# Optimization experiments

Measured on AMD Instinct MI355X. Metric: run time of the kernel, lower is better.

Reference implementation:

```python
import jax, jax.numpy as jnp
import numpy as np

B, N, K, D, H, FF, L, NH = 8, 50, 20, 3, 128, 2048, 3, 8
S = N * K
HD = H // NH


def setup_inputs() -> dict:
    key = jax.random.key(0)
    ks = jax.random.split(key, 16)
    visited = jax.random.uniform(ks[0], (B, S)) < 0.05
    # the single most-recent action per batch row (status flips 0 -> 1)
    action_idx = jax.random.randint(ks[1], (B,), 0, S)
    visited = visited.at[jnp.arange(B), action_idx].set(True)
    feats = jax.random.normal(ks[2], (B, S, D - 1)) * visited[:, :, None]
    state = jnp.concatenate([feats, visited[:, :, None].astype(jnp.float32)], axis=-1)
    prev_state = state.at[jnp.arange(B), action_idx, :].set(0.0)

    def w(k, shape, s=0.02):
        return jax.random.normal(k, shape, dtype=jnp.float32) * s

    return dict(
        prev_state=prev_state, state=state,
        W_pre=w(ks[3], (D, H)), b_pre=jnp.zeros(H),
        Wq=w(ks[4], (L, H, H)), bq=jnp.zeros((L, H)),
        Wk=w(ks[5], (L, H, H)), bk=jnp.zeros((L, H)),
        Wv=w(ks[6], (L, H, H)), bv=jnp.zeros((L, H)),
        Wo=w(ks[7], (L, H, H)), bo=jnp.zeros((L, H)),
        ln1_g=jnp.ones((L, H)), ln1_b=jnp.zeros((L, H)),
        Wff1=w(ks[8], (L, H, FF)), bff1=jnp.zeros((L, FF)),
        Wff2=w(ks[9], (L, FF, H)), bff2=jnp.zeros((L, H)),
        ln2_g=jnp.ones((L, H)), ln2_b=jnp.zeros((L, H)),
        W_comb=w(ks[10], (2 * H, H)), b_comb=jnp.zeros(H),
        W_dec=w(ks[11], (H, H)), b_dec=jnp.zeros(H),
        W_lin=w(ks[12], (S, S)), b_lin=jnp.zeros(S),
    )


def _layer_norm(x, g, b, eps=1e-5):
    m = jnp.mean(x, -1, keepdims=True)
    v = jnp.mean(jnp.square(x - m), -1, keepdims=True)
    return (x - m) * jax.lax.rsqrt(v + eps) * g + b


def _update_mask(state):
    # vectorized equivalent of the original Python-loop scatter mask
    status = state[:, :, -1] != 0                      # visited [B, S], S = K*N channel-major
    mask = status
    vis_kn = status.reshape(B, K, N)
    user_any = vis_kn.any(axis=1)                      # [B, N]: user visited on any channel
    mask = mask | jnp.broadcast_to(user_any[:, None, :], (B, K, N)).reshape(B, S)
    assigned = state.reshape(B, K, N, D).sum(-1) != 0  # [B, K, N]
    full = assigned.sum(-1) >= 2                       # [B, K]: channel already has 2 users
    mask = mask | jnp.broadcast_to(full[:, :, None], (B, K, N)).reshape(B, S)
    return mask


def reference(prev_state, state, W_pre, b_pre, Wq, bq, Wk, bk, Wv, bv, Wo, bo,
              ln1_g, ln1_b, Wff1, bff1, Wff2, bff2, ln2_g, ln2_b,
              W_comb, b_comb, W_dec, b_dec, W_lin, b_lin):
    mask = _update_mask(state)
    # exactly one status change per batch row (sequential RL step)
    diff = prev_state[:, :, -1] != state[:, :, -1]
    act_idx = jnp.argmax(diff, axis=1)                 # [B]

    x = state @ W_pre + b_pre                          # [B, S, H]
    scale = np.float32(1.0 / np.sqrt(HD))
    for i in range(L):  # 3 post-LN transformer encoder layers
        q = (x @ Wq[i] + bq[i]).reshape(B, S, NH, HD)
        k = (x @ Wk[i] + bk[i]).reshape(B, S, NH, HD)
        v = (x @ Wv[i] + bv[i]).reshape(B, S, NH, HD)
        att = jax.nn.softmax(jnp.einsum('bqhd,bkhd->bhqk', q, k) * scale, axis=-1)
        o = jnp.einsum('bhqk,bkhd->bqhd', att, v).reshape(B, S, H) @ Wo[i] + bo[i]
        x = _layer_norm(x + o, ln1_g[i], ln1_b[i])
        ff = jax.nn.relu(x @ Wff1[i] + bff1[i]) @ Wff2[i] + bff2[i]
        x = _layer_norm(x + ff, ln2_g[i], ln2_b[i])

    last = x[jnp.arange(B), act_idx]                   # [B, H]
    combined = jnp.concatenate([x.mean(axis=1), last], axis=-1)  # [B, 2H]
    g = combined @ W_comb + b_comb                     # [B, H]
    dec = x @ W_dec + b_dec                            # [B, S, H]
    scores = jnp.einsum('bsh,bh->bs', dec, g)          # [B, S]
    masked = scores @ W_lin + b_lin                    # Q-Learning head
    return jnp.where(mask, -jnp.inf, masked)
```

## Files before the change

### kernel.cpp

```cpp
#include <hip/hip_runtime.h>
#include <math.h>

#define Bb 8
#define Ss 1000
#define Kk 20
#define Nn 50
#define Dd 3
#define Hh 128
#define FFf 2048
#define Ll 3
#define NHh 8
#define HDd 16
#define ROWS (Bb*Ss)

#define SENTINEL -3.0e38f

typedef unsigned short ush;
typedef short short8 __attribute__((ext_vector_type(8)));
typedef float f32x4 __attribute__((ext_vector_type(4)));

__device__ __forceinline__ ush f2b(float f) {
  unsigned x = __float_as_uint(f);
  return (ush)((x + 0x7fff + ((x >> 16) & 1)) >> 16);
}

__global__ __launch_bounds__(256) void mask_kernel(const float* __restrict__ state,
                                                   const float* __restrict__ prev_state,
                                                   int* __restrict__ mask, int* __restrict__ act_idx) {
  int b = blockIdx.x, tid = threadIdx.x;
  __shared__ unsigned char status[Ss], assigned[Ss], uany[Nn], fullk[Kk];
  __shared__ int act;
  if (tid == 0) act = 1 << 30;
  __syncthreads();
  for (int s = tid; s < Ss; s += 256) {
    const float* st = state + ((size_t)b * Ss + s) * Dd;
    float f2 = st[2];
    status[s] = (f2 != 0.f);
    assigned[s] = ((st[0] + st[1] + f2) != 0.f);
    float p2 = prev_state[((size_t)b * Ss + s) * Dd + 2];
    if (p2 != f2) atomicMin(&act, s);
  }
  __syncthreads();
  if (tid < Nn) {
    unsigned char a = 0;
    for (int k = 0; k < Kk; ++k) a |= status[k * Nn + tid];
    uany[tid] = a;
  } else if (tid >= 64 && tid < 64 + Kk) {
    int k = tid - 64, cnt = 0;
    for (int n = 0; n < Nn; ++n) cnt += assigned[k * Nn + n];
    fullk[k] = (cnt >= 2);
  }
  __syncthreads();
  for (int s = tid; s < Ss; s += 256)
    mask[b * Ss + s] = (int)(status[s] | uany[s % Nn] | fullk[s / Nn]);
  if (tid == 0) act_idx[b] = (act >= Ss) ? 0 : act;
}

__global__ __launch_bounds__(256) void pre_kernel(const float* __restrict__ state,
                                                  const float* __restrict__ W_pre,
                                                  const float* __restrict__ b_pre,
                                                  float* __restrict__ x, ush* __restrict__ xbf) {
  int idx = blockIdx.x * 256 + threadIdx.x;
  if (idx >= ROWS * Hh) return;
  int row = idx >> 7, n = idx & 127;
  const float* st = state + (size_t)row * Dd;
  float v = b_pre[n] + st[0] * W_pre[n] + st[1] * W_pre[Hh + n] + st[2] * W_pre[2 * Hh + n];
  x[idx] = v;
  xbf[idx] = f2b(v);
}

#define S1 (384*128)
#define S2 (128*128)
#define S3 (2048*128)
#define S4 (128*2048)
#define SPL (S1+S2+S3+S4)
__global__ __launch_bounds__(256) void wprep_kernel(const float* __restrict__ Wq, const float* __restrict__ Wk,
                                                    const float* __restrict__ Wv, const float* __restrict__ Wo,
                                                    const float* __restrict__ Wff1, const float* __restrict__ Wff2,
                                                    const float* __restrict__ bq, const float* __restrict__ bk,
                                                    const float* __restrict__ bv, const float* __restrict__ W_dec,
                                                    ush* __restrict__ wqkvT, ush* __restrict__ woT,
                                                    ush* __restrict__ wff1T, ush* __restrict__ wff2T,
                                                    float* __restrict__ bqkv, float* __restrict__ wdecT) {
  int idx = blockIdx.x * 256 + threadIdx.x;
  if (idx < Ll * SPL) {
    int l = idx / SPL, r = idx % SPL;
    if (r < S1) {
      int k = r / 384, n = r % 384;
      float v = (n < 128) ? Wq[((size_t)l * Hh + k) * Hh + n]
              : (n < 256) ? Wk[((size_t)l * Hh + k) * Hh + (n - 128)]
                          : Wv[((size_t)l * Hh + k) * Hh + (n - 256)];
      wqkvT[((size_t)l * 384 + n) * 128 + k] = f2b(v);
    } else if (r < S1 + S2) {
      int rr = r - S1; int k = rr >> 7, n = rr & 127;
      woT[((size_t)l * 128 + n) * 128 + k] = f2b(Wo[((size_t)l * Hh + k) * Hh + n]);
    } else if (r < S1 + S2 + S3) {
      int rr = r - S1 - S2; int k = rr >> 11, n = rr & 2047;
      wff1T[((size_t)l * 2048 + n) * 128 + k] = f2b(Wff1[((size_t)l * Hh + k) * FFf + n]);
    } else {
      int rr = r - S1 - S2 - S3; int k = rr >> 7, n = rr & 127;
      wff2T[((size_t)l * 128 + n) * 2048 + k] = f2b(Wff2[((size_t)l * FFf + k) * Hh + n]);
    }
  }
  if (idx < Ll * 384) {
    int l = idx / 384, c = idx % 384;
    bqkv[idx] = (c < 128) ? bq[l * Hh + c] : (c < 256 ? bk[l * Hh + c - 128] : bv[l * Hh + c - 256]);
  }
  if (idx < Hh * Hh) {
    int k = idx >> 7, n = idx & 127;
    wdecT[(size_t)n * Hh + k] = W_dec[idx];
  }
}

#define LDP 40
template <int RELU, int QKVV>
__global__ __launch_bounds__(256) void gemm_mfma(const ush* __restrict__ A, const ush* __restrict__ Wt,
                                                 const float* __restrict__ bias, ush* __restrict__ out,
                                                 int N, int K, ush* __restrict__ vTout) {
  __shared__ ush As[2][64 * LDP];
  __shared__ ush Bs[2][64 * LDP];
  int tid = threadIdx.x;
  int lane = tid & 63, wid = tid >> 6;
  int wr = wid >> 1, wc = wid & 1;
  int m0 = blockIdx.y * 64, n0 = blockIdx.x * 64;
  int lrow = tid >> 2, lk = (tid & 3) << 3;
  int quad = lane >> 4, l16 = lane & 15, kb = quad << 3;

  const ush* Ap = A + (size_t)(m0 + lrow) * K + lk;
  const ush* Bp = Wt + (size_t)(n0 + lrow) * K + lk;

  f32x4 acc[2][2];
#pragma unroll
  for (int i = 0; i < 2; ++i)
#pragma unroll
    for (int j = 0; j < 2; ++j) acc[i][j] = (f32x4){0.f, 0.f, 0.f, 0.f};

  short8 pa = *(const short8*)Ap;
  short8 pb = *(const short8*)Bp;
  *(short8*)&As[0][lrow * LDP + lk] = pa;
  *(short8*)&Bs[0][lrow * LDP + lk] = pb;
  __syncthreads();

  int NT = K >> 5;
  for (int it = 0; it < NT; ++it) {
    int cur = it & 1;
    bool have = (it + 1 < NT);
    if (have) {
      pa = *(const short8*)(Ap + (it + 1) * 32);
      pb = *(const short8*)(Bp + (it + 1) * 32);
    }
    short8 a0 = *(short8*)&As[cur][(wr * 32 + l16) * LDP + kb];
    short8 a1 = *(short8*)&As[cur][(wr * 32 + 16 + l16) * LDP + kb];
    short8 b0 = *(short8*)&Bs[cur][(wc * 32 + l16) * LDP + kb];
    short8 b1 = *(short8*)&Bs[cur][(wc * 32 + 16 + l16) * LDP + kb];
    acc[0][0] = __builtin_amdgcn_mfma_f32_16x16x32_bf16(a0, b0, acc[0][0], 0, 0, 0);
    acc[0][1] = __builtin_amdgcn_mfma_f32_16x16x32_bf16(a0, b1, acc[0][1], 0, 0, 0);
    acc[1][0] = __builtin_amdgcn_mfma_f32_16x16x32_bf16(a1, b0, acc[1][0], 0, 0, 0);
    acc[1][1] = __builtin_amdgcn_mfma_f32_16x16x32_bf16(a1, b1, acc[1][1], 0, 0, 0);
    if (have) {
      *(short8*)&As[cur ^ 1][lrow * LDP + lk] = pa;
      *(short8*)&Bs[cur ^ 1][lrow * LDP + lk] = pb;
    }
    __syncthreads();
  }

#pragma unroll
  for (int i = 0; i < 2; ++i)
#pragma unroll
    for (int j = 0; j < 2; ++j) {
      int col = n0 + wc * 32 + j * 16 + l16;
      int rbase = m0 + wr * 32 + i * 16 + quad * 4;
      float bval = bias[col];
#pragma unroll
      for (int v = 0; v < 4; ++v) {
        float o = acc[i][j][v] + bval;
        if (RELU) o = fmaxf(o, 0.f);
        if (QKVV && col >= 256) {
          int row = rbase + v;
          int bb2 = row / 1000, qq = row - bb2 * 1000;
          vTout[((size_t)(bb2 * 128 + (col - 256))) * 1024 + qq] = f2b(o);
        } else {
          out[(size_t)(rbase + v) * N + col] = f2b(o);
        }
      }
    }
}

#define F2P 72
template <int KK>
__global__ __launch_bounds__(256) void gemm_ln_kernel(const ush* __restrict__ A,
                                                      const ush* __restrict__ Wt,
                                                      const float* __restrict__ bias,
                                                      const float* __restrict__ ln_g, const float* __restrict__ ln_b,
                                                      float* __restrict__ x, ush* __restrict__ xbf) {
  __shared__ ush As[2][32 * F2P];
  __shared__ ush Bs[2][128 * F2P];
  __shared__ float red1[2][2][16], red2[2][2][16];
  __shared__ float pbias[128], pg[128], pb[128];

  int tid = threadIdx.x, lane = tid & 63, w = tid >> 6;
  int wr = w & 1, wc = w >> 1;
  int l16 = lane & 15, quad = lane >> 4, kb = quad * 8;
  int m0 = blockIdx.x * 32;
  if (tid < 128) { pbias[tid] = bias[tid]; pg[tid] = ln_g[tid]; pb[tid] = ln_b[tid]; }

  f32x4 acc[4];
#pragma unroll
  for (int j = 0; j < 4; ++j) acc[j] = (f32x4){0.f, 0.f, 0.f, 0.f};

  int arow = tid >> 3, alk = (tid & 7) << 3;
  const ush* Ap = A + (size_t)(m0 + arow) * KK + alk;
  const ush* Bp = Wt + (size_t)arow * KK + alk;

  short8 pa = *(const short8*)Ap;
  short8 pbr[4];
#pragma unroll
  for (int rep = 0; rep < 4; ++rep)
    pbr[rep] = *(const short8*)(Bp + (size_t)rep * 32 * KK);
  *(short8*)&As[0][arow * F2P + alk] = pa;
#pragma unroll
  for (int rep = 0; rep < 4; ++rep)
    *(short8*)&Bs[0][(rep * 32 + arow) * F2P + alk] = pbr[rep];
  __syncthreads();

  const int NT = KK / 64;
  for (int it = 0; it < NT; ++it) {
    int cur = it & 1;
    bool have = (it + 1 < NT);
    if (have) {
      pa = *(const short8*)(Ap + (it + 1) * 64);
#pragma unroll
      for (int rep = 0; rep < 4; ++rep)
        pbr[rep] = *(const short8*)(Bp + (size_t)rep * 32 * KK + (it + 1) * 64);
    }
#pragma unroll
    for (int kk = 0; kk < 2; ++kk) {
      short8 a = *(short8*)&As[cur][(wr * 16 + l16) * F2P + kk * 32 + kb];
#pragma unroll
      for (int j = 0; j < 4; ++j) {
        short8 b = *(short8*)&Bs[cur][(wc * 64 + j * 16 + l16) * F2P + kk * 32 + kb];
        acc[j] = __builtin_amdgcn_mfma_f32_16x16x32_bf16(a, b, acc[j], 0, 0, 0);
      }
    }
    if (have) {
      *(short8*)&As[cur ^ 1][arow * F2P + alk] = pa;
#pragma unroll
      for (int rep = 0; rep < 4; ++rep)
        *(short8*)&Bs[cur ^ 1][(rep * 32 + arow) * F2P + alk] = pbr[rep];
    }
    __syncthreads();
  }

  float v[4][4], s1[4] = {0.f, 0.f, 0.f, 0.f}, s2[4] = {0.f, 0.f, 0.f, 0.f};
#pragma unroll
  for (int j = 0; j < 4; ++j) {
    int col = wc * 64 + j * 16 + l16;
#pragma unroll
    for (int r = 0; r < 4; ++r) {
      int row = m0 + wr * 16 + quad * 4 + r;
      float vv = acc[j][r] + pbias[col] + x[(size_t)row * Hh + col];
      v[j][r] = vv; s1[r] += vv; s2[r] += vv * vv;
    }
  }
#pragma unroll
  for (int m = 1; m <= 8; m <<= 1) {
#pragma unroll
    for (int r = 0; r < 4; ++r) { s1[r] += __shfl_xor(s1[r], m); s2[r] += __shfl_xor(s2[r], m); }
  }
  if (l16 == 0) {
#pragma unroll
    for (int r = 0; r < 4; ++r) {
      red1[wr][wc][quad * 4 + r] = s1[r];
      red2[wr][wc][quad * 4 + r] = s2[r];
    }
  }
  __syncthreads();
#pragma unroll
  for (int r = 0; r < 4; ++r) {
    int qr = quad * 4 + r;
    float t1 = red1[wr][0][qr] + red1[wr][1][qr];
    float t2 = red2[wr][0][qr] + red2[wr][1][qr];
    float mean = t1 * (1.f / 128.f);
    float var = t2 * (1.f / 128.f) - mean * mean;
    float rstd = rsqrtf(var + 1e-5f);
    int row = m0 + wr * 16 + quad * 4 + r;
#pragma unroll
    for (int j = 0; j < 4; ++j) {
      int col = wc * 64 + j * 16 + l16;
      float o = (v[j][r] - mean) * rstd * pg[col] + pb[col];
      size_t gi = (size_t)row * Hh + col;
      x[gi] = o; xbf[gi] = f2b(o);
    }
  }
}

__global__ __launch_bounds__(256) void attn_mfma(const ush* __restrict__ qkv,
                                                 const ush* __restrict__ vT,
                                                 ush* __restrict__ attn_o) {
  int blk = blockIdx.x;
  int local = blk >> 3;
  int bh = ((blk & 7) << 3) | (local >> 4);
  int qt = local & 15;
  int b = bh >> 3, h = bh & 7;
  int qbase = qt * 64;
  int tid = threadIdx.x, lane = tid & 63, w = tid >> 6;
  int l16 = lane & 15, quad = lane >> 4, kb = quad * 8;

  __shared__ ush Ks[2][64][40];
  __shared__ ush Vs[2][16][72];
  __shared__ ush Pb[4][16][72];

  if (tid < 128) {
    int row = tid >> 1, g = tid & 1;
    *(short8*)&Ks[0][row][16 + g * 8] = (short8){0, 0, 0, 0, 0, 0, 0, 0};
    *(short8*)&Ks[1][row][16 + g * 8] = (short8){0, 0, 0, 0, 0, 0, 0, 0};
  }

  int qrow = qbase + w * 16 + l16; if (qrow >= Ss) qrow = Ss - 1;
  short8 aq = *(const short8*)(qkv + (size_t)(b * Ss + qrow) * 384 + h * HDd + kb);

  int srow = tid >> 1, sg = tid & 1;
  int sd = (tid - 128) >> 3, skg = (tid - 128) & 7;
  const ush* kbase = qkv + (size_t)b * Ss * 384 + 128 + h * HDd;
  const ush* vbase = vT + (size_t)(b * 128 + h * 16) * 1024;

  if (tid < 128) {
    short8 s8 = (short8){0, 0, 0, 0, 0, 0, 0, 0};
    if (srow < Ss) s8 = *(const short8*)(kbase + (size_t)srow * 384 + sg * 8);
    *(short8*)&Ks[0][srow][sg * 8] = s8;
  } else {
    *(short8*)&Vs[0][sd][skg * 8] = *(const short8*)(vbase + (size_t)sd * 1024 + skg * 8);
  }
  __syncthreads();

  const short one_b = (short)0x3F80;
  const short8 ones = (short8){one_b, one_b, one_b, one_b, one_b, one_b, one_b, one_b};
  f32x4 acc_pv = (f32x4){0.f, 0.f, 0.f, 0.f};
  f32x4 acc_l = (f32x4){0.f, 0.f, 0.f, 0.f};
  const f32x4 zero4 = (f32x4){0.f, 0.f, 0.f, 0.f};

  for (int it = 0; it < 16; ++it) {
    int k0 = it * 64;
    int cur = it & 1, nxt = cur ^ 1;
    bool have = (it + 1 < 16);

    short8 gk, gv;
    if (have) {
      if (tid < 128) {
        gk = (short8){0, 0, 0, 0, 0, 0, 0, 0};
        int key = k0 + 64 + srow;
        if (key < Ss) gk = *(const short8*)(kbase + (size_t)key * 384 + sg * 8);
      } else {
        gv = *(const short8*)(vbase + (size_t)sd * 1024 + k0 + 64 + skg * 8);
      }
    }

    bool tail = (k0 + 64 > Ss);
#pragma unroll
    for (int kn = 0; kn < 4; ++kn) {
      short8 ak = *(short8*)&Ks[cur][kn * 16 + l16][kb];
      f32x4 s = __builtin_amdgcn_mfma_f32_16x16x32_bf16(ak, aq, zero4, 0, 0, 0);
      float p0 = __expf(s[0] * 0.25f);
      float p1 = __expf(s[1] * 0.25f);
      float p2 = __expf(s[2] * 0.25f);
      float p3 = __expf(s[3] * 0.25f);
      if (tail) {
        int keyb = k0 + kn * 16 + quad * 4;
        if (keyb + 0 >= Ss) p0 = 0.f;
        if (keyb + 1 >= Ss) p1 = 0.f;
        if (keyb + 2 >= Ss) p2 = 0.f;
        if (keyb + 3 >= Ss) p3 = 0.f;
      }
      unsigned lo, hi;
      asm("v_cvt_pk_bf16_f32 %0, %1, %2" : "=v"(lo) : "v"(p0), "v"(p1));
      asm("v_cvt_pk_bf16_f32 %0, %1, %2" : "=v"(hi) : "v"(p2), "v"(p3));
      *(uint2*)&Pb[w][l16][kn * 16 + quad * 4] = make_uint2(lo, hi);
    }

    short8 pa0 = *(short8*)&Pb[w][l16][kb];
    short8 pa1 = *(short8*)&Pb[w][l16][32 + kb];
    short8 vb0 = *(short8*)&Vs[cur][l16][kb];
    short8 vb1 = *(short8*)&Vs[cur][l16][32 + kb];
    acc_pv = __builtin_amdgcn_mfma_f32_16x16x32_bf16(pa0, vb0, acc_pv, 0, 0, 0);
    acc_pv = __builtin_amdgcn_mfma_f32_16x16x32_bf16(pa1, vb1, acc_pv, 0, 0, 0);
    acc_l = __builtin_amdgcn_mfma_f32_16x16x32_bf16(pa0, ones, acc_l, 0, 0, 0);
    acc_l = __builtin_amdgcn_mfma_f32_16x16x32_bf16(pa1, ones, acc_l, 0, 0, 0);

    if (have) {
      if (tid < 128) *(short8*)&Ks[nxt][srow][sg * 8] = gk;
      else *(short8*)&Vs[nxt][sd][skg * 8] = gv;
    }
    __syncthreads();
  }

#pragma unroll
  for (int r = 0; r < 4; ++r) {
    int q = qbase + w * 16 + quad * 4 + r;
    if (q < Ss)
      attn_o[((size_t)(b * Ss + q)) * Hh + h * HDd + l16] = f2b(acc_pv[r] / acc_l[r]);
  }
}

__global__ __launch_bounds__(128) void mean_part_kernel(const float* __restrict__ x,
                                                        float* __restrict__ mpart) {
  int c = blockIdx.x, b = blockIdx.y, n = threadIdx.x;
  const float* xb = x + ((size_t)b * Ss + c * 125) * Hh + n;
  float s = 0.f;
#pragma unroll 5
  for (int i = 0; i < 125; ++i) s += xb[(size_t)i * Hh];
  mpart[(c * Bb + b) * Hh + n] = s;
}

__global__ __launch_bounds__(128) void ghc_kernel(const float* __restrict__ x, const float* __restrict__ mpart,
                                                  const int* __restrict__ act_idx,
                                                  const float* __restrict__ W_comb, const float* __restrict__ b_comb,
                                                  const float* __restrict__ wdecT, const float* __restrict__ b_dec,
                                                  float* __restrict__ h, float* __restrict__ cb) {
  int b = blockIdx.x, n = threadIdx.x;
  __shared__ float cs[2 * Hh], gs[Hh], red[2];
  float mean = 0.f;
#pragma unroll
  for (int c = 0; c < 8; ++c) mean += mpart[(c * Bb + b) * Hh + n];
  cs[n] = mean * (1.f / Ss);
  cs[Hh + n] = x[((size_t)b * Ss + act_idx[b]) * Hh + n];
  __syncthreads();
  float acc = b_comb[n];
  for (int j = 0; j < 2 * Hh; ++j) acc += cs[j] * W_comb[(size_t)j * Hh + n];
  gs[n] = acc;
  __syncthreads();
  float hv = 0.f;
  for (int c = 0; c < Hh; ++c) hv += wdecT[(size_t)c * Hh + n] * gs[c];
  h[b * Hh + n] = hv;
  float t = b_dec[n] * gs[n];
  for (int off = 32; off; off >>= 1) t += __shfl_down(t, off);
  if ((n & 63) == 0) red[n >> 6] = t;
  __syncthreads();
  if (n == 0) cb[b] = red[0] + red[1];
}

__global__ __launch_bounds__(256) void scores_kernel(const float* __restrict__ x, const float* __restrict__ h,
                                                     const float* __restrict__ cb, float* __restrict__ scores) {
  int wid = threadIdx.x >> 6, lane = threadIdx.x & 63;
  int row = blockIdx.x * 4 + wid;
  if (row >= ROWS) return;
  int b = row / Ss;
  const float* xr = x + (size_t)row * Hh;
  const float* hb = h + b * Hh;
  float s = xr[lane] * hb[lane] + xr[lane + 64] * hb[lane + 64];
  for (int off = 32; off; off >>= 1) s += __shfl_down(s, off);
  if (lane == 0) scores[row] = s + cb[b];
}

__global__ __launch_bounds__(256) void final_part(const float* __restrict__ scores,
                                                  const float* __restrict__ W_lin,
                                                  float* __restrict__ fpart) {
  int spc = blockIdx.x, kc = blockIdx.y;
  int tid = threadIdx.x;
  __shared__ float ss[8][125];
  for (int i = tid; i < 8 * 125; i += 256) {
    int bb = i / 125, s = i - bb * 125;
    ss[bb][s] = scores[bb * Ss + kc * 125 + s];
  }
  __syncthreads();
  if (tid < 250) {
    int sp = spc * 250 + tid;
    float acc[8];
#pragma unroll
    for (int bb = 0; bb < 8; ++bb) acc[bb] = 0.f;
    const float* wl = &W_lin[(size_t)(kc * 125) * Ss + sp];
#pragma unroll 5
    for (int s = 0; s < 125; ++s) {
      float wv = wl[(size_t)s * Ss];
#pragma unroll
      for (int bb = 0; bb < 8; ++bb) acc[bb] = fmaf(ss[bb][s], wv, acc[bb]);
    }
#pragma unroll
    for (int bb = 0; bb < 8; ++bb)
      fpart[((size_t)kc * Bb + bb) * Ss + sp] = acc[bb];
  }
}

__global__ __launch_bounds__(256) void final_combine(const float* __restrict__ fpart,
                                                     const float* __restrict__ b_lin,
                                                     const int* __restrict__ mask,
                                                     float* __restrict__ out) {
  int b = blockIdx.y;
  int sp = blockIdx.x * 256 + threadIdx.x;
  if (sp >= Ss) return;
  float acc = b_lin[sp];
#pragma unroll
  for (int kc = 0; kc < 8; ++kc) acc += fpart[((size_t)kc * Bb + b) * Ss + sp];
  out[b * Ss + sp] = mask[b * Ss + sp] ? SENTINEL : acc;
}

extern "C" void kernel_launch(void* const* d_in, const int* in_sizes, int n_in,
                              void* d_out, int out_size, void* d_ws, size_t ws_size,
                              hipStream_t stream) {
  const float* prev_state = (const float*)d_in[0];
  const float* state = (const float*)d_in[1];
  const float* W_pre = (const float*)d_in[2];
  const float* b_pre = (const float*)d_in[3];
  const float* Wq = (const float*)d_in[4];
  const float* bq = (const float*)d_in[5];
  const float* Wk = (const float*)d_in[6];
  const float* bk = (const float*)d_in[7];
  const float* Wv = (const float*)d_in[8];
  const float* bv = (const float*)d_in[9];
  const float* Wo = (const float*)d_in[10];
  const float* bo = (const float*)d_in[11];
  const float* ln1_g = (const float*)d_in[12];
  const float* ln1_b = (const float*)d_in[13];
  const float* Wff1 = (const float*)d_in[14];
  const float* bff1 = (const float*)d_in[15];
  const float* Wff2 = (const float*)d_in[16];
  const float* bff2 = (const float*)d_in[17];
  const float* ln2_g = (const float*)d_in[18];
  const float* ln2_b = (const float*)d_in[19];
  const float* W_comb = (const float*)d_in[20];
  const float* b_comb = (const float*)d_in[21];
  const float* W_dec = (const float*)d_in[22];
  const float* b_dec = (const float*)d_in[23];
  const float* W_lin = (const float*)d_in[24];
  const float* b_lin = (const float*)d_in[25];

  char* wsp = (char*)d_ws;
  auto alloc = [&](size_t bytes) { char* p = wsp; wsp += (bytes + 255) & ~(size_t)255; return p; };
  int* mask = (int*)alloc(ROWS * 4);
  int* act = (int*)alloc(Bb * 4);
  ush* wqkvT = (ush*)alloc((size_t)Ll * 384 * 128 * 2);
  ush* woT = (ush*)alloc((size_t)Ll * 128 * 128 * 2);
  ush* wff1T = (ush*)alloc((size_t)Ll * 2048 * 128 * 2);
  ush* wff2T = (ush*)alloc((size_t)Ll * 128 * 2048 * 2);
  float* bqkv = (float*)alloc((size_t)Ll * 384 * 4);
  float* wdecT = (float*)alloc((size_t)Hh * Hh * 4);
  float* x = (float*)alloc((size_t)ROWS * Hh * 4);
  ush* xbf = (ush*)alloc((size_t)ROWS * Hh * 2);
  ush* qkv_bf = (ush*)alloc((size_t)ROWS * 384 * 2);
  ush* vT = (ush*)alloc((size_t)Bb * 128 * 1024 * 2);
  ush* attn_ob = (ush*)alloc((size_t)ROWS * Hh * 2);
  float* mpart = (float*)alloc((size_t)8 * Bb * Hh * 4);
  float* hbuf = (float*)alloc((size_t)Bb * Hh * 4);
  float* cb = (float*)alloc((size_t)Bb * 4);
  float* scores = (float*)alloc((size_t)ROWS * 4);
  float* fpart = (float*)alloc((size_t)8 * Bb * Ss * 4);
  ush* ffb = (ush*)alloc((size_t)ROWS * FFf * 2);

  wprep_kernel<<<dim3((Ll * SPL + 255) / 256), 256, 0, stream>>>(Wq, Wk, Wv, Wo, Wff1, Wff2, bq, bk, bv, W_dec,
                                                                 wqkvT, woT, wff1T, wff2T, bqkv, wdecT);
  mask_kernel<<<Bb, 256, 0, stream>>>(state, prev_state, mask, act);
  pre_kernel<<<dim3((ROWS * Hh + 255) / 256), 256, 0, stream>>>(state, W_pre, b_pre, x, xbf);

  for (int l = 0; l < Ll; ++l) {
    gemm_mfma<0, 1><<<dim3(384 / 64, ROWS / 64), 256, 0, stream>>>(
        xbf, wqkvT + (size_t)l * 384 * 128, bqkv + l * 384, qkv_bf, 384, 128, vT);
    attn_mfma<<<dim3(1024), 256, 0, stream>>>(qkv_bf, vT, attn_ob);
    gemm_ln_kernel<128><<<dim3(ROWS / 32), 256, 0, stream>>>(
        attn_ob, woT + (size_t)l * 128 * 128, bo + l * Hh, ln1_g + l * Hh, ln1_b + l * Hh, x, xbf);
    gemm_mfma<1, 0><<<dim3(2048 / 64, ROWS / 64), 256, 0, stream>>>(
        xbf, wff1T + (size_t)l * 2048 * 128, bff1 + l * FFf, ffb, 2048, 128, nullptr);
    gemm_ln_kernel<2048><<<dim3(ROWS / 32), 256, 0, stream>>>(
        ffb, wff2T + (size_t)l * 128 * 2048, bff2 + l * Hh, ln2_g + l * Hh, ln2_b + l * Hh, x, xbf);
  }

  mean_part_kernel<<<dim3(8, Bb), 128, 0, stream>>>(x, mpart);
  ghc_kernel<<<Bb, 128, 0, stream>>>(x, mpart, act, W_comb, b_comb, wdecT, b_dec, hbuf, cb);
  scores_kernel<<<dim3(ROWS / 4), 256, 0, stream>>>(x, hbuf, cb, scores);
  final_part<<<dim3(4, 8), 256, 0, stream>>>(scores, W_lin, fpart);
  final_combine<<<dim3(4, Bb), 256, 0, stream>>>(fpart, b_lin, mask, (float*)d_out);
}
```

Before: 381.2 us.

## Tile weight transposes, vectorize V^T stores, add 16-row out-proj LN kernel, fuse mean

New measurement: 383.5 us. About the same (+0.6%).

```diff
diff --git a/kernel.cpp b/kernel.cpp
--- a/kernel.cpp
+++ b/kernel.cpp
@@ -17,6 +17,7 @@
 
 typedef unsigned short ush;
 typedef short short8 __attribute__((ext_vector_type(8)));
+typedef short short4v __attribute__((ext_vector_type(4)));
 typedef float f32x4 __attribute__((ext_vector_type(4)));
 
 __device__ __forceinline__ ush f2b(float f) {
@@ -59,9 +60,11 @@
 __global__ __launch_bounds__(256) void pre_kernel(const float* __restrict__ state,
                                                   const float* __restrict__ W_pre,
                                                   const float* __restrict__ b_pre,
-                                                  float* __restrict__ x, ush* __restrict__ xbf) {
+                                                  float* __restrict__ x, ush* __restrict__ xbf,
+                                                  float* __restrict__ mpart) {
   int idx = blockIdx.x * 256 + threadIdx.x;
   if (idx >= ROWS * Hh) return;
+  if (idx < Bb * Hh) mpart[idx] = 0.f;
   int row = idx >> 7, n = idx & 127;
   const float* st = state + (size_t)row * Dd;
   float v = b_pre[n] + st[0] * W_pre[n] + st[1] * W_pre[Hh + n] + st[2] * W_pre[2 * Hh + n];
@@ -69,46 +72,67 @@
   xbf[idx] = f2b(v);
 }
 
-#define S1 (384*128)
-#define S2 (128*128)
-#define S3 (2048*128)
-#define S4 (128*2048)
-#define SPL (S1+S2+S3+S4)
-__global__ __launch_bounds__(256) void wprep_kernel(const float* __restrict__ Wq, const float* __restrict__ Wk,
-                                                    const float* __restrict__ Wv, const float* __restrict__ Wo,
-                                                    const float* __restrict__ Wff1, const float* __restrict__ Wff2,
-                                                    const float* __restrict__ bq, const float* __restrict__ bk,
-                                                    const float* __restrict__ bv, const float* __restrict__ W_dec,
-                                                    ush* __restrict__ wqkvT, ush* __restrict__ woT,
-                                                    ush* __restrict__ wff1T, ush* __restrict__ wff2T,
-                                                    float* __restrict__ bqkv, float* __restrict__ wdecT) {
-  int idx = blockIdx.x * 256 + threadIdx.x;
-  if (idx < Ll * SPL) {
-    int l = idx / SPL, r = idx % SPL;
-    if (r < S1) {
-      int k = r / 384, n = r % 384;
-      float v = (n < 128) ? Wq[((size_t)l * Hh + k) * Hh + n]
-              : (n < 256) ? Wk[((size_t)l * Hh + k) * Hh + (n - 128)]
-                          : Wv[((size_t)l * Hh + k) * Hh + (n - 256)];
-      wqkvT[((size_t)l * 384 + n) * 128 + k] = f2b(v);
-    } else if (r < S1 + S2) {
-      int rr = r - S1; int k = rr >> 7, n = rr & 127;
-      woT[((size_t)l * 128 + n) * 128 + k] = f2b(Wo[((size_t)l * Hh + k) * Hh + n]);
-    } else if (r < S1 + S2 + S3) {
-      int rr = r - S1 - S2; int k = rr >> 11, n = rr & 2047;
-      wff1T[((size_t)l * 2048 + n) * 128 + k] = f2b(Wff1[((size_t)l * Hh + k) * FFf + n]);
-    } else {
-      int rr = r - S1 - S2 - S3; int k = rr >> 7, n = rr & 127;
-      wff2T[((size_t)l * 128 + n) * 2048 + k] = f2b(Wff2[((size_t)l * FFf + k) * Hh + n]);
-    }
-  }
-  if (idx < Ll * 384) {
-    int l = idx / 384, c = idx % 384;
-    bqkv[idx] = (c < 128) ? bq[l * Hh + c] : (c < 256 ? bk[l * Hh + c - 128] : bv[l * Hh + c - 256]);
-  }
-  if (idx < Hh * Hh) {
-    int k = idx >> 7, n = idx & 127;
-    wdecT[(size_t)n * Hh + k] = W_dec[idx];
+#define TQKV 144
+#define TWO  48
+#define TFF1 768
+#define TFF2 768
+#define TWD  16
+#define TBIAS 5
+#define TTOT (TQKV+TWO+TFF1+TFF2+TWD+TBIAS)
+__global__ __launch_bounds__(256) void transpose_prep(
+    const float* __restrict__ Wq, const float* __restrict__ Wk, const float* __restrict__ Wv,
+    const float* __restrict__ Wo, const float* __restrict__ Wff1, const float* __restrict__ Wff2,
+    const float* __restrict__ bq, const float* __restrict__ bk, const float* __restrict__ bv,
+    const float* __restrict__ W_dec,
+    ush* __restrict__ wqkvT, ush* __restrict__ woT, ush* __restrict__ wff1T, ush* __restrict__ wff2T,
+    float* __restrict__ bqkv, float* __restrict__ wdecT) {
+  int t = blockIdx.x, tid = threadIdx.x;
+  if (t >= TTOT - TBIAS) {
+    int idx = (t - (TTOT - TBIAS)) * 256 + tid;
+    if (idx < Ll * 384) {
+      int l = idx / 384, c = idx % 384;
+      bqkv[idx] = (c < 128) ? bq[l * Hh + c] : (c < 256 ? bk[l * Hh + c - 128] : bv[l * Hh + c - 256]);
+    }
+    return;
+  }
+  __shared__ float lf[32][33];
+  int tr = tid >> 5, tc = tid & 31;
+  const float* s; ush* d = nullptr; float* df = nullptr;
+  int sp, dp;
+  if (t < TQKV) {
+    int l = t / 48, rem = t % 48, mat = rem / 16, tt = rem % 16;
+    int ti = tt >> 2, tj = tt & 3;
+    const float* m = (mat == 0) ? Wq : (mat == 1) ? Wk : Wv;
+    s = m + (size_t)l * 16384 + (size_t)(ti * 32) * 128 + tj * 32; sp = 128;
+    d = wqkvT + ((size_t)l * 384 + mat * 128 + tj * 32) * 128 + ti * 32; dp = 128;
+  } else if (t < TQKV + TWO) {
+    int r0 = t - TQKV; int l = r0 / 16, tt = r0 % 16, ti = tt >> 2, tj = tt & 3;
+    s = Wo + (size_t)l * 16384 + (size_t)(ti * 32) * 128 + tj * 32; sp = 128;
+    d = woT + ((size_t)l * 128 + tj * 32) * 128 + ti * 32; dp = 128;
+  } else if (t < TQKV + TWO + TFF1) {
+    int r0 = t - TQKV - TWO; int l = r0 / 256, tt = r0 % 256, ti = tt >> 6, tj = tt & 63;
+    s = Wff1 + (size_t)l * 128 * 2048 + (size_t)(ti * 32) * 2048 + tj * 32; sp = 2048;
+    d = wff1T + ((size_t)l * 2048 + tj * 32) * 128 + ti * 32; dp = 128;
+  } else if (t < TQKV + TWO + TFF1 + TFF2) {
+    int r0 = t - TQKV - TWO - TFF1; int l = r0 / 256, tt = r0 % 256, ti = tt >> 2, tj = tt & 3;
+    s = Wff2 + (size_t)l * 2048 * 128 + (size_t)(ti * 32) * 128 + tj * 32; sp = 128;
+    d = wff2T + ((size_t)l * 128 + tj * 32) * 2048 + ti * 32; dp = 2048;
+  } else {
+    int tt = t - TQKV - TWO - TFF1 - TFF2; int ti = tt >> 2, tj = tt & 3;
+    s = W_dec + (size_t)(ti * 32) * 128 + tj * 32; sp = 128;
+    df = wdecT + (size_t)(tj * 32) * 128 + ti * 32; dp = 128;
+  }
+#pragma unroll
+  for (int p = 0; p < 4; ++p) {
+    int r = tr + p * 8;
+    lf[r][tc] = s[(size_t)r * sp + tc];
+  }
+  __syncthreads();
+#pragma unroll
+  for (int p = 0; p < 4; ++p) {
+    int r = tr + p * 8;
+    if (d) d[(size_t)r * dp + tc] = f2b(lf[tc][r]);
+    else   df[(size_t)r * dp + tc] = lf[tc][r];
   }
 }
 
@@ -171,15 +195,17 @@
       int col = n0 + wc * 32 + j * 16 + l16;
       int rbase = m0 + wr * 32 + i * 16 + quad * 4;
       float bval = bias[col];
-#pragma unroll
-      for (int v = 0; v < 4; ++v) {
-        float o = acc[i][j][v] + bval;
-        if (RELU) o = fmaxf(o, 0.f);
-        if (QKVV && col >= 256) {
-          int row = rbase + v;
-          int bb2 = row / 1000, qq = row - bb2 * 1000;
-          vTout[((size_t)(bb2 * 128 + (col - 256))) * 1024 + qq] = f2b(o);
-        } else {
+      if (QKVV && col >= 256) {
+        int bb2 = rbase / 1000, qq = rbase - bb2 * 1000;
+        short4v pk;
+#pragma unroll
+        for (int v = 0; v < 4; ++v) pk[v] = (short)f2b(acc[i][j][v] + bval);
+        *(short4v*)&vTout[((size_t)(bb2 * 128 + (col - 256))) * 1024 + qq] = pk;
+      } else {
+#pragma unroll
+        for (int v = 0; v < 4; ++v) {
+          float o = acc[i][j][v] + bval;
+          if (RELU) o = fmaxf(o, 0.f);
           out[(size_t)(rbase + v) * N + col] = f2b(o);
         }
       }
@@ -187,12 +213,14 @@
 }
 
 #define F2P 72
-template <int KK>
+template <int MEANOUT>
 __global__ __launch_bounds__(256) void gemm_ln_kernel(const ush* __restrict__ A,
                                                       const ush* __restrict__ Wt,
                                                       const float* __restrict__ bias,
                                                       const float* __restrict__ ln_g, const float* __restrict__ ln_b,
-                                                      float* __restrict__ x, ush* __restrict__ xbf) {
+                                                      float* __restrict__ x, ush* __restrict__ xbf,
+                                                      float* __restrict__ mpart) {
+  const int KK = 2048;
   __shared__ ush As[2][32 * F2P];
   __shared__ ush Bs[2][128 * F2P];
   __shared__ float red1[2][2][16], red2[2][2][16];
@@ -275,6 +303,7 @@
     }
   }
   __syncthreads();
+  float osum[4] = {0.f, 0.f, 0.f, 0.f};
 #pragma unroll
   for (int r = 0; r < 4; ++r) {
     int qr = quad * 4 + r;
@@ -287,6 +316,117 @@
 #pragma unroll
     for (int j = 0; j < 4; ++j) {
       int col = wc * 64 + j * 16 + l16;
+      float o = (v[j][r] - mean) * rstd * pg[col] + pb[col];
+      size_t gi = (size_t)row * Hh + col;
+      x[gi] = o; xbf[gi] = f2b(o);
+      if (MEANOUT) osum[j] += o;
+    }
+  }
+  if (MEANOUT) {
+    int gb = (m0 + wr * 16 + quad * 4) / 1000;
+#pragma unroll
+    for (int j = 0; j < 4; ++j)
+      atomicAdd(&mpart[gb * 128 + wc * 64 + j * 16 + l16], osum[j]);
+  }
+}
+
+__global__ __launch_bounds__(256) void gemm_ln16(const ush* __restrict__ A,
+                                                 const ush* __restrict__ Wt,
+                                                 const float* __restrict__ bias,
+                                                 const float* __restrict__ ln_g, const float* __restrict__ ln_b,
+                                                 float* __restrict__ x, ush* __restrict__ xbf) {
+  __shared__ ush As[2][16 * F2P];
+  __shared__ ush Bs[2][128 * F2P];
+  __shared__ float red1[4][16], red2[4][16];
+  __shared__ float pbias[128], pg[128], pb[128];
+
+  int tid = threadIdx.x, lane = tid & 63, w = tid >> 6;
+  int l16 = lane & 15, quad = lane >> 4, kb = quad * 8;
+  int m0 = blockIdx.x * 16;
+  if (tid < 128) { pbias[tid] = bias[tid]; pg[tid] = ln_g[tid]; pb[tid] = ln_b[tid]; }
+
+  f32x4 acc[2];
+  acc[0] = (f32x4){0.f, 0.f, 0.f, 0.f};
+  acc[1] = (f32x4){0.f, 0.f, 0.f, 0.f};
+
+  int srow = tid >> 3, slk = (tid & 7) << 3;
+  const ush* Ap = A + (size_t)(m0 + srow) * 128 + slk;
+  const ush* Bp = Wt + (size_t)srow * 128 + slk;
+
+  short8 pa;
+  short8 pbr[4];
+  if (tid < 128) pa = *(const short8*)Ap;
+#pragma unroll
+  for (int rep = 0; rep < 4; ++rep)
+    pbr[rep] = *(const short8*)(Bp + (size_t)rep * 32 * 128);
+  if (tid < 128) *(short8*)&As[0][srow * F2P + slk] = pa;
+#pragma unroll
+  for (int rep = 0; rep < 4; ++rep)
+    *(short8*)&Bs[0][(rep * 32 + srow) * F2P + slk] = pbr[rep];
+  __syncthreads();
+
+#pragma unroll
+  for (int it = 0; it < 2; ++it) {
+    if (it == 0) {
+      if (tid < 128) pa = *(const short8*)(Ap + 64);
+#pragma unroll
+      for (int rep = 0; rep < 4; ++rep)
+        pbr[rep] = *(const short8*)(Bp + (size_t)rep * 32 * 128 + 64);
+    }
+#pragma unroll
+    for (int kk = 0; kk < 2; ++kk) {
+      short8 a = *(short8*)&As[it][l16 * F2P + kk * 32 + kb];
+#pragma unroll
+      for (int j = 0; j < 2; ++j) {
+        short8 b = *(short8*)&Bs[it][(w * 32 + j * 16 + l16) * F2P + kk * 32 + kb];
+        acc[j] = __builtin_amdgcn_mfma_f32_16x16x32_bf16(a, b, acc[j], 0, 0, 0);
+      }
+    }
+    if (it == 0) {
+      if (tid < 128) *(short8*)&As[1][srow * F2P + slk] = pa;
+#pragma unroll
+      for (int rep = 0; rep < 4; ++rep)
+        *(short8*)&Bs[1][(rep * 32 + srow) * F2P + slk] = pbr[rep];
+    }
+    __syncthreads();
+  }
+
+  float v[2][4], s1[4] = {0.f, 0.f, 0.f, 0.f}, s2[4] = {0.f, 0.f, 0.f, 0.f};
+#pragma unroll
+  for (int j = 0; j < 2; ++j) {
+    int col = w * 32 + j * 16 + l16;
+#pragma unroll
+    for (int r = 0; r < 4; ++r) {
+      int row = m0 + quad * 4 + r;
+      float vv = acc[j][r] + pbias[col] + x[(size_t)row * Hh + col];
+      v[j][r] = vv; s1[r] += vv; s2[r] += vv * vv;
+    }
+  }
+#pragma unroll
+  for (int m = 1; m <= 8; m <<= 1) {
+#pragma unroll
+    for (int r = 0; r < 4; ++r) { s1[r] += __shfl_xor(s1[r], m); s2[r] += __shfl_xor(s2[r], m); }
+  }
+  if (l16 == 0) {
+#pragma unroll
+    for (int r = 0; r < 4; ++r) {
+      red1[w][quad * 4 + r] = s1[r];
+      red2[w][quad * 4 + r] = s2[r];
+    }
+  }
+  __syncthreads();
+#pragma unroll
+  for (int r = 0; r < 4; ++r) {
+    int qr = quad * 4 + r;
+    float t1 = red1[0][qr] + red1[1][qr] + red1[2][qr] + red1[3][qr];
+    float t2 = red2[0][qr] + red2[1][qr] + red2[2][qr] + red2[3][qr];
+    float mean = t1 * (1.f / 128.f);
+    float var = t2 * (1.f / 128.f) - mean * mean;
+    float rstd = rsqrtf(var + 1e-5f);
+    int row = m0 + qr;
+#pragma unroll
+    for (int j = 0; j < 2; ++j) {
+      int col = w * 32 + j * 16 + l16;
       float o = (v[j][r] - mean) * rstd * pg[col] + pb[col];
       size_t gi = (size_t)row * Hh + col;
       x[gi] = o; xbf[gi] = f2b(o);
@@ -401,16 +541,6 @@
   }
 }
 
-__global__ __launch_bounds__(128) void mean_part_kernel(const float* __restrict__ x,
-                                                        float* __restrict__ mpart) {
-  int c = blockIdx.x, b = blockIdx.y, n = threadIdx.x;
-  const float* xb = x + ((size_t)b * Ss + c * 125) * Hh + n;
-  float s = 0.f;
-#pragma unroll 5
-  for (int i = 0; i < 125; ++i) s += xb[(size_t)i * Hh];
-  mpart[(c * Bb + b) * Hh + n] = s;
-}
-
 __global__ __launch_bounds__(128) void ghc_kernel(const float* __restrict__ x, const float* __restrict__ mpart,
                                                   const int* __restrict__ act_idx,
                                                   const float* __restrict__ W_comb, const float* __restrict__ b_comb,
@@ -418,10 +548,7 @@
                                                   float* __restrict__ h, float* __restrict__ cb) {
   int b = blockIdx.x, n = threadIdx.x;
   __shared__ float cs[2 * Hh], gs[Hh], red[2];
-  float mean = 0.f;
-#pragma unroll
-  for (int c = 0; c < 8; ++c) mean += mpart[(c * Bb + b) * Hh + n];
-  cs[n] = mean * (1.f / Ss);
+  cs[n] = mpart[b * Hh + n] * (1.f / Ss);
   cs[Hh + n] = x[((size_t)b * Ss + act_idx[b]) * Hh + n];
   __syncthreads();
   float acc = b_comb[n];
@@ -538,31 +665,34 @@
   ush* qkv_bf = (ush*)alloc((size_t)ROWS * 384 * 2);
   ush* vT = (ush*)alloc((size_t)Bb * 128 * 1024 * 2);
   ush* attn_ob = (ush*)alloc((size_t)ROWS * Hh * 2);
-  float* mpart = (float*)alloc((size_t)8 * Bb * Hh * 4);
+  float* mpart = (float*)alloc((size_t)Bb * Hh * 4);
   float* hbuf = (float*)alloc((size_t)Bb * Hh * 4);
   float* cb = (float*)alloc((size_t)Bb * 4);
   float* scores = (float*)alloc((size_t)ROWS * 4);
   float* fpart = (float*)alloc((size_t)8 * Bb * Ss * 4);
   ush* ffb = (ush*)alloc((size_t)ROWS * FFf * 2);
 
-  wprep_kernel<<<dim3((Ll * SPL + 255) / 256), 256, 0, stream>>>(Wq, Wk, Wv, Wo, Wff1, Wff2, bq, bk, bv, W_dec,
-                                                                 wqkvT, woT, wff1T, wff2T, bqkv, wdecT);
+  transpose_prep<<<dim3(TTOT), 256, 0, stream>>>(Wq, Wk, Wv, Wo, Wff1, Wff2, bq, bk, bv, W_dec,
+                                                 wqkvT, woT, wff1T, wff2T, bqkv, wdecT);
   mask_kernel<<<Bb, 256, 0, stream>>>(state, prev_state, mask, act);
-  pre_kernel<<<dim3((ROWS * Hh + 255) / 256), 256, 0, stream>>>(state, W_pre, b_pre, x, xbf);
+  pre_kernel<<<dim3((ROWS * Hh + 255) / 256), 256, 0, stream>>>(state, W_pre, b_pre, x, xbf, mpart);
 
   for (int l = 0; l < Ll; ++l) {
     gemm_mfma<0, 1><<<dim3(384 / 64, ROWS / 64), 256, 0, stream>>>(
         xbf, wqkvT + (size_t)l * 384 * 128, bqkv + l * 384, qkv_bf, 384, 128, vT);
     attn_mfma<<<dim3(1024), 256, 0, stream>>>(qkv_bf, vT, attn_ob);
-    gemm_ln_kernel<128><<<dim3(ROWS / 32), 256, 0, stream>>>(
+    gemm_ln16<<<dim3(ROWS / 16), 256, 0, stream>>>(
         attn_ob, woT + (size_t)l * 128 * 128, bo + l * Hh, ln1_g + l * Hh, ln1_b + l * Hh, x, xbf);
     gemm_mfma<1, 0><<<dim3(2048 / 64, ROWS / 64), 256, 0, stream>>>(
         xbf, wff1T + (size_t)l * 2048 * 128, bff1 + l * FFf, ffb, 2048, 128, nullptr);
-    gemm_ln_kernel<2048><<<dim3(ROWS / 32), 256, 0, stream>>>(
-        ffb, wff2T + (size_t)l * 128 * 2048, bff2 + l * Hh, ln2_g + l * Hh, ln2_b + l * Hh, x, xbf);
-  }
-
-  mean_part_kernel<<<dim3(8, Bb), 128, 0, stream>>>(x, mpart);
+    if (l == Ll - 1)
+      gemm_ln_kernel<1><<<dim3(ROWS / 32), 256, 0, stream>>>(
+          ffb, wff2T + (size_t)l * 128 * 2048, bff2 + l * Hh, ln2_g + l * Hh, ln2_b + l * Hh, x, xbf, mpart);
+    else
+      gemm_ln_kernel<0><<<dim3(ROWS / 32), 256, 0, stream>>>(
+          ffb, wff2T + (size_t)l * 128 * 2048, bff2 + l * Hh, ln2_g + l * Hh, ln2_b + l * Hh, x, xbf, mpart);
+  }
+
   ghc_kernel<<<Bb, 128, 0, stream>>>(x, mpart, act, W_comb, b_comb, wdecT, b_dec, hbuf, cb);
   scores_kernel<<<dim3(ROWS / 4), 256, 0, stream>>>(x, hbuf, cb, scores);
   final_part<<<dim3(4, 8), 256, 0, stream>>>(scores, W_lin, fpart);
```
